# Kernel tuning notes

Measured on AMD Instinct MI355X. Metric: run time of the kernel, lower is better.

The kernel has to match this reference:

```python
import jax, jax.numpy as jnp
import numpy as np

B, C, CK, CV, W, H = 8, 256, 256, 256, 64, 64
EPS = 1e-6

def setup_inputs() -> dict:
    key = jax.random.key(0)
    ks = jax.random.split(key, 13)
    def wmat(k, shape, fan_in):
        return jax.random.normal(k, shape, jnp.float32) / np.float32(np.sqrt(fan_in))
    return {
        "x": jax.random.normal(ks[0], (B, C, W, H), jnp.float32),
        "qw": wmat(ks[1], (CK, C), C), "qb": jnp.zeros((CK,), jnp.float32),
        "kw": wmat(ks[2], (CK, C), C), "kb": jnp.zeros((CK,), jnp.float32),
        "vw": wmat(ks[3], (CV, C), C), "vb": jnp.zeros((CV,), jnp.float32),
        "rw": wmat(ks[4], (C, CV), CV), "rb": jnp.zeros((C,), jnp.float32),
        "c1w": wmat(ks[5], (C, C, 3, 3), C * 9), "c1b": jnp.zeros((C,), jnp.float32),
        "c2w": wmat(ks[6], (C, C, 3, 3), C * 9), "c2b": jnp.zeros((C,), jnp.float32),
    }

def reference(x, qw, qb, kw, kb, vw, vb, rw, rb, c1w, c1b, c2w, c2b):
    Bz, Cc, Wd, Hd = x.shape
    n = Wd * Hd
    xf = x.reshape(Bz, Cc, n)                                  # [b,c,n]
    Q = jnp.einsum('oc,bcn->bon', qw, xf) + qb[None, :, None]  # 1x1 conv
    K = jnp.einsum('oc,bcn->bon', kw, xf) + kb[None, :, None]
    V = jnp.einsum('oc,bcn->bon', vw, xf) + vb[None, :, None]
    # l2 norm over channel dim (per token), exactly as torch.norm(dim=-2)
    Qn = Q / jnp.linalg.norm(Q, axis=1, keepdims=True)
    Kn = K / jnp.linalg.norm(K, axis=1, keepdims=True)
    Qt = jnp.transpose(Qn, (0, 2, 1))                          # [b,n,ck]
    # head loops in the original sum over the full channel dim -> single einsum
    agg_dom = jnp.einsum('bnk,bk->bn', Qt, Kn.sum(-1))         # [b,n]
    denom = 1.0 / (n + agg_dom + EPS)                          # [b,n]
    vsum = V.sum(-1)                                           # [b,cv]
    kv = jnp.einsum('bkn,bcn->bkc', Kn, V)                     # K^T V, [b,ck,cv]
    qkv = jnp.einsum('bnk,bkc->bcn', Qt, kv)                   # [b,cv,n]
    wv = (vsum[:, :, None] + qkv) * denom[:, None, :]
    wv = wv.reshape(Bz, -1, Hd, Wd)                            # matches torch .view(b,cv,h,w)
    attn = jnp.einsum('oc,bchw->bohw', rw, wv) + rb[None, :, None, None]
    dn = ('NCHW', 'OIHW', 'NCHW')
    h = jax.lax.conv_general_dilated(attn, c1w, (1, 1), 'SAME', dimension_numbers=dn) + c1b[None, :, None, None]
    h = jax.lax.conv_general_dilated(h, c2w, (1, 1), 'SAME', dimension_numbers=dn) + c2b[None, :, None, None]
    return h * x + x
```

## Files before the change

### kernel.cpp

```cpp
#include <hip/hip_runtime.h>
#include <math.h>


typedef unsigned short u16;
typedef __attribute__((ext_vector_type(8))) short short8;
typedef __attribute__((ext_vector_type(4))) float f32x4;
typedef __attribute__((ext_vector_type(4))) unsigned short us4v;

#define ASYNC16(g, l) __builtin_amdgcn_global_load_lds( \
    (const __attribute__((address_space(1))) unsigned int*)(g), \
    (__attribute__((address_space(3))) unsigned int*)(l), 16, 0, 0)

static __device__ __forceinline__ float b2f(u16 h) {
  unsigned int u = ((unsigned int)h) << 16;
  return __builtin_bit_cast(float, u);
}
static __device__ __forceinline__ u16 f2b(float f) {
  unsigned int u = __builtin_bit_cast(unsigned int, f);
  u += 0x7fffu + ((u >> 16) & 1u);
  return (u16)(u >> 16);
}

#define NB 1048576L

__global__ __launch_bounds__(256) void prep1(
    const float* __restrict__ qw, const float* __restrict__ kw,
    const float* __restrict__ vw, const float* __restrict__ rw,
    const float* __restrict__ c1w, const float* __restrict__ c2w,
    const float* __restrict__ kb, const float* __restrict__ vb,
    u16* __restrict__ qw16, u16* __restrict__ kvw16, u16* __restrict__ rwT16,
    u16* __restrict__ wr1, u16* __restrict__ wr2,
    float* __restrict__ kvbias, float* __restrict__ zbuf)
{
  if (blockIdx.x == 5632) {
    int t = threadIdx.x;
    if (t < 256) { kvbias[t] = kb[t]; kvbias[t + 256] = vb[t]; }
    if (t < 64) zbuf[t] = 0.f;
    return;
  }
  long g = (long)blockIdx.x * 256 + threadIdx.x;
  if (g < 65536) {
    qw16[g] = f2b(qw[g]);
  } else if (g < 196608) {
    long e = g - 65536;
    kvw16[e] = f2b(e < 65536 ? kw[e] : vw[e - 65536]);
  } else if (g < 262144) {
    long e = g - 196608;
    int cv = e >> 8, co = e & 255;
    rwT16[e] = f2b(rw[co * 256 + cv]);
  } else if (g < 851968) {
    long e = g - 262144;
    int m = e / 2304, r = e - m * 2304;
    int d = r >> 8, c = r & 255;
    wr1[e] = f2b(c1w[m * 2304 + c * 9 + d]);
  } else {
    long e = g - 851968;
    int m = e / 2304, r = e - m * 2304;
    int d = r >> 8, c = r & 255;
    wr2[e] = f2b(c2w[m * 2304 + c * 9 + d]);
  }
}

__global__ __launch_bounds__(256) void prep_T(
    const float* __restrict__ c1w, const float* __restrict__ rb, float* __restrict__ T)
{
  int m = blockIdx.x, co = threadIdx.x;
  float r = rb[co];
  const float* p = c1w + (long)m * 2304 + co * 9;
  float lv[9];
#pragma unroll
  for (int d = 0; d < 9; d++) lv[d] = p[d] * r;
#pragma unroll
  for (int d = 0; d < 9; d++)
#pragma unroll
    for (int off = 32; off; off >>= 1) lv[d] += __shfl_down(lv[d], off, 64);
  __shared__ float red[4][9];
  int w = co >> 6, l = co & 63;
  if (l == 0)
#pragma unroll
    for (int d = 0; d < 9; d++) red[w][d] = lv[d];
  __syncthreads();
  if (co < 9) T[m * 9 + co] = red[0][co] + red[1][co] + red[2][co] + red[3][co];
}

__global__ __launch_bounds__(256) void corr_k(
    const float* __restrict__ T, const float* __restrict__ c1b, float* __restrict__ corr)
{
  int e = blockIdx.x * 256 + threadIdx.x;
  int m = e & 255, p = e >> 8;
  int y = p >> 6, xx = p & 63;
  float s = c1b[m];
#pragma unroll
  for (int d = 0; d < 9; d++) {
    int dy = d / 3 - 1, dx = d - (d / 3) * 3 - 1;
    if ((unsigned)(y + dy) < 64u && (unsigned)(xx + dx) < 64u) s += T[m * 9 + d];
  }
  corr[e] = s;
}

__global__ __launch_bounds__(256) void transposeX(
    const float* __restrict__ x, u16* __restrict__ xT)
{
  __shared__ float T[64][65];
  int n0 = blockIdx.x * 64, c0 = blockIdx.y * 64, b = blockIdx.z;
  int t = threadIdx.x;
#pragma unroll
  for (int i = 0; i < 4; i++) {
    int c = (t >> 4) + i * 16, nn = (t & 15) * 4;
    float4 v = *(const float4*)&x[(long)b * NB + (long)(c0 + c) * 4096 + n0 + nn];
    T[c][nn] = v.x; T[c][nn + 1] = v.y; T[c][nn + 2] = v.z; T[c][nn + 3] = v.w;
  }
  __syncthreads();
#pragma unroll
  for (int i = 0; i < 4; i++) {
    int n = (t >> 4) + i * 16, cc = (t & 15) * 4;
    us4v o;
#pragma unroll
    for (int e = 0; e < 4; e++) o[e] = f2b(T[cc + e][n]);
    *(us4v*)&xT[(long)b * NB + (long)(n0 + n) * 256 + c0 + cc] = o;
  }
}

__global__ __launch_bounds__(256) void gemm_nt(
    const u16* __restrict__ A, const u16* __restrict__ B, u16* __restrict__ out,
    int K, int lda, int ldb, long sAb, long sBb, long sOb, long sR, long sC,
    int mode, const float* __restrict__ p1, const float* __restrict__ p2)
{
  __shared__ __align__(16) u16 As[2][128 * 32];
  __shared__ __align__(16) u16 Bs[2][128 * 32];
  int b = blockIdx.z;
  long i0 = (long)blockIdx.y * 128;
  long j0 = (long)blockIdx.x * 128;
  const u16* Ab = A + b * sAb + i0 * lda;
  const u16* Bb = B + b * sBb + j0 * ldb;
  int t = threadIdx.x, wave = t >> 6, lane = t & 63;
  int wi = (wave >> 1) * 64, wj = (wave & 1) * 64;
  int li = lane & 15, quad = lane >> 4;
  int qs = (lane & 3) ^ ((lane >> 3) & 3);
  int qx = quad ^ ((lane >> 1) & 3);
  int r0 = (wave * 128 + lane) >> 2;
  int r1 = (wave * 128 + 64 + lane) >> 2;
  f32x4 acc[4][4];
#pragma unroll
  for (int i = 0; i < 4; i++)
#pragma unroll
    for (int j = 0; j < 4; j++) acc[i][j] = (f32x4){0.f, 0.f, 0.f, 0.f};

  auto STAGE = [&](int kc, int buf) {
    int k0 = kc * 32;
    ASYNC16(Ab + (long)r0 * lda + k0 + qs * 8, &As[buf][(wave * 128) * 8]);
    ASYNC16(Bb + (long)r0 * ldb + k0 + qs * 8, &Bs[buf][(wave * 128) * 8]);
    ASYNC16(Ab + (long)r1 * lda + k0 + qs * 8, &As[buf][(wave * 128 + 64) * 8]);
    ASYNC16(Bb + (long)r1 * ldb + k0 + qs * 8, &Bs[buf][(wave * 128 + 64) * 8]);
  };

  int nk = K >> 5, cur = 0;
  STAGE(0, 0);
#pragma unroll 1
  for (int kc = 0; kc < nk; kc++) {
    if (kc + 1 < nk) {
      STAGE(kc + 1, cur ^ 1);
      asm volatile("s_waitcnt vmcnt(4)" ::: "memory");
    } else {
      asm volatile("s_waitcnt vmcnt(0)" ::: "memory");
    }
    __builtin_amdgcn_s_barrier();
    const u16* as = &As[cur][0];
    const u16* bs = &Bs[cur][0];
    short8 af[4], bf[4];
#pragma unroll
    for (int s = 0; s < 4; s++) af[s] = *(const short8*)&as[(wi + s * 16 + li) * 32 + qx * 8];
#pragma unroll
    for (int s = 0; s < 4; s++) bf[s] = *(const short8*)&bs[(wj + s * 16 + li) * 32 + qx * 8];
#pragma unroll
    for (int si = 0; si < 4; si++)
#pragma unroll
      for (int sj = 0; sj < 4; sj++)
        acc[si][sj] = __builtin_amdgcn_mfma_f32_16x16x32_bf16(af[si], bf[sj], acc[si][sj], 0, 0, 0);
    __builtin_amdgcn_s_barrier();
    cur ^= 1;
  }

#pragma unroll
  for (int si = 0; si < 4; si++)
#pragma unroll
    for (int sj = 0; sj < 4; sj++) {
      long col = j0 + wj + sj * 16 + li;
#pragma unroll
      for (int r = 0; r < 4; r++) {
        long row = i0 + wi + si * 16 + quad * 4 + r;
        float v = acc[si][sj][r];
        if (mode == 0) {
          if (p1) v += p1[row];
          if (p2) v += p2[col];
        } else {
          v = (v + p1[b * 256 + col]) * p2[b * 4096 + row];
        }
        out[b * sOb + row * sR + col * sC] = f2b(v);
      }
    }
}

__global__ __launch_bounds__(256) void gemm_kv(
    const u16* __restrict__ KV, float* __restrict__ part)
{
  __shared__ __align__(16) u16 As[2][128 * 32];
  __shared__ __align__(16) u16 Bs[2][128 * 32];
  int z = blockIdx.z;
  int b = z & 7, sp = z >> 3;
  long i0 = (long)blockIdx.y * 128;
  long j0 = (long)blockIdx.x * 128;
  const u16* Ab = KV + (long)b * 2 * NB + i0 * 4096;
  const u16* Bb = KV + (long)b * 2 * NB + NB + j0 * 4096;
  int t = threadIdx.x, wave = t >> 6, lane = t & 63;
  int wi = (wave >> 1) * 64, wj = (wave & 1) * 64;
  int li = lane & 15, quad = lane >> 4;
  int qs = (lane & 3) ^ ((lane >> 3) & 3);
  int qx = quad ^ ((lane >> 1) & 3);
  int r0 = (wave * 128 + lane) >> 2;
  int r1 = (wave * 128 + 64 + lane) >> 2;
  f32x4 acc[4][4];
#pragma unroll
  for (int i = 0; i < 4; i++)
#pragma unroll
    for (int j = 0; j < 4; j++) acc[i][j] = (f32x4){0.f, 0.f, 0.f, 0.f};

  auto STAGE = [&](int kc, int buf) {
    int k0 = sp * 512 + kc * 32;
    ASYNC16(Ab + (long)r0 * 4096 + k0 + qs * 8, &As[buf][(wave * 128) * 8]);
    ASYNC16(Bb + (long)r0 * 4096 + k0 + qs * 8, &Bs[buf][(wave * 128) * 8]);
    ASYNC16(Ab + (long)r1 * 4096 + k0 + qs * 8, &As[buf][(wave * 128 + 64) * 8]);
    ASYNC16(Bb + (long)r1 * 4096 + k0 + qs * 8, &Bs[buf][(wave * 128 + 64) * 8]);
  };

  int cur = 0;
  STAGE(0, 0);
#pragma unroll 1
  for (int kc = 0; kc < 16; kc++) {
    if (kc + 1 < 16) {
      STAGE(kc + 1, cur ^ 1);
      asm volatile("s_waitcnt vmcnt(4)" ::: "memory");
    } else {
      asm volatile("s_waitcnt vmcnt(0)" ::: "memory");
    }
    __builtin_amdgcn_s_barrier();
    const u16* as = &As[cur][0];
    const u16* bs = &Bs[cur][0];
    short8 af[4], bf[4];
#pragma unroll
    for (int s = 0; s < 4; s++) af[s] = *(const short8*)&as[(wi + s * 16 + li) * 32 + qx * 8];
#pragma unroll
    for (int s = 0; s < 4; s++) bf[s] = *(const short8*)&bs[(wj + s * 16 + li) * 32 + qx * 8];
#pragma unroll
    for (int si = 0; si < 4; si++)
#pragma unroll
      for (int sj = 0; sj < 4; sj++)
        acc[si][sj] = __builtin_amdgcn_mfma_f32_16x16x32_bf16(af[si], bf[sj], acc[si][sj], 0, 0, 0);
    __builtin_amdgcn_s_barrier();
    cur ^= 1;
  }

  float* outp = part + ((long)sp * 8 + b) * 65536;
#pragma unroll
  for (int si = 0; si < 4; si++)
#pragma unroll
    for (int sj = 0; sj < 4; sj++) {
      long col = j0 + wj + sj * 16 + li;
#pragma unroll
      for (int r = 0; r < 4; r++) {
        long row = i0 + wi + si * 16 + quad * 4 + r;
        outp[col * 256 + row] = acc[si][sj][r];
      }
    }
}

__global__ __launch_bounds__(256) void reduce_kv(
    const float* __restrict__ part, u16* __restrict__ kvT)
{
  int g = blockIdx.x * 256 + threadIdx.x;
  float s = 0.f;
#pragma unroll
  for (int sp = 0; sp < 8; sp++) s += part[(long)sp * 524288 + g];
  kvT[g] = f2b(s);
}

__global__ __launch_bounds__(256) void normQden(
    u16* __restrict__ Qt, const float* __restrict__ ksum, float* __restrict__ den)
{
  int row = blockIdx.x * 4 + (threadIdx.x >> 6);
  int lane = threadIdx.x & 63;
  int b = row >> 12;
  u16* p = Qt + (long)row * 256 + lane * 4;
  us4v v = *(const us4v*)p;
  float f0 = b2f(v[0]), f1 = b2f(v[1]), f2 = b2f(v[2]), f3 = b2f(v[3]);
  float s = f0 * f0 + f1 * f1 + f2 * f2 + f3 * f3;
#pragma unroll
  for (int m = 32; m; m >>= 1) s += __shfl_xor(s, m, 64);
  float r = 1.0f / sqrtf(s);
  float o0 = f0 * r, o1 = f1 * r, o2 = f2 * r, o3 = f3 * r;
  us4v o;
  o[0] = f2b(o0); o[1] = f2b(o1); o[2] = f2b(o2); o[3] = f2b(o3);
  *(us4v*)p = o;
  float4 ks = *(const float4*)&ksum[b * 256 + lane * 4];
  float s2 = o0 * ks.x + o1 * ks.y + o2 * ks.z + o3 * ks.w;
#pragma unroll
  for (int m = 32; m; m >>= 1) s2 += __shfl_xor(s2, m, 64);
  if (lane == 0) den[row] = 1.0f / (4096.0f + s2 + 1e-6f);
}

__global__ __launch_bounds__(256) void sumsqK(
    const u16* __restrict__ KV, float* __restrict__ rsqK)
{
  __shared__ float red[16][68];
  int b = blockIdx.x >> 6, nc = blockIdx.x & 63;
  int n0 = nc * 64;
  int t = threadIdx.x;
  int nn = (t & 15) * 4, cg = t >> 4;
  const u16* base = KV + (long)b * 2 * NB;
  float s0 = 0.f, s1 = 0.f, s2 = 0.f, s3 = 0.f;
  for (int st = 0; st < 16; st++) {
    int c = cg + st * 16;
    us4v v = *(const us4v*)(base + (long)c * 4096 + n0 + nn);
    float a = b2f(v[0]), bb = b2f(v[1]), cc = b2f(v[2]), dd = b2f(v[3]);
    s0 = fmaf(a, a, s0); s1 = fmaf(bb, bb, s1);
    s2 = fmaf(cc, cc, s2); s3 = fmaf(dd, dd, s3);
  }
  red[cg][nn] = s0; red[cg][nn + 1] = s1; red[cg][nn + 2] = s2; red[cg][nn + 3] = s3;
  __syncthreads();
  if (t < 64) {
    float s = 0.f;
#pragma unroll
    for (int g = 0; g < 16; g++) s += red[g][t];
    rsqK[b * 4096 + n0 + t] = 1.0f / sqrtf(s);
  }
}

__global__ __launch_bounds__(256) void scale_sums(
    u16* __restrict__ KV, const float* __restrict__ rsqK,
    float* __restrict__ ksum, float* __restrict__ vsum)
{
  int z = blockIdx.x;
  int isV = z >> 11, rem = z & 2047, b = rem >> 8, c = rem & 255;
  u16* row = KV + (long)b * 2 * NB + (long)isV * NB + (long)c * 4096;
  const float* rq = rsqK + b * 4096;
  int t = threadIdx.x;
  float s = 0.f;
  short8 v0 = *(const short8*)&row[t * 16];
  short8 v1 = *(const short8*)&row[t * 16 + 8];
  if (!isV) {
    short8 o0, o1;
#pragma unroll
    for (int e = 0; e < 8; e++) {
      float a = b2f((u16)v0[e]) * rq[t * 16 + e];
      float bb = b2f((u16)v1[e]) * rq[t * 16 + 8 + e];
      s += a + bb;
      o0[e] = (short)f2b(a); o1[e] = (short)f2b(bb);
    }
    *(short8*)&row[t * 16] = o0;
    *(short8*)&row[t * 16 + 8] = o1;
  } else {
#pragma unroll
    for (int e = 0; e < 8; e++) s += b2f((u16)v0[e]) + b2f((u16)v1[e]);
  }
#pragma unroll
  for (int off = 32; off; off >>= 1) s += __shfl_down(s, off, 64);
  __shared__ float red[4];
  if ((t & 63) == 0) red[t >> 6] = s;
  __syncthreads();
  if (t == 0)
    (isV ? vsum : ksum)[b * 256 + c] = red[0] + red[1] + red[2] + red[3];
}

__global__ __launch_bounds__(512, 2) void conv_gemm(
    const u16* __restrict__ inT, const u16* __restrict__ wr,
    const float* __restrict__ cb, const float* __restrict__ xres,
    const float* __restrict__ zbuf,
    u16* __restrict__ out16, float* __restrict__ out32, int mode)
{
  __shared__ __align__(16) u16 S[2 * 24576];

  int lin = blockIdx.x;
  int b   = lin & 7;
  int n0  = (lin >> 3) * 128;

  int t = threadIdx.x, wave = t >> 6, lane = t & 63;
  int wm = (wave >> 1) * 64, wn = (wave & 1) * 64;
  int li = lane & 15, quad = lane >> 4;
  int qs8 = (lane & 7) ^ ((lane >> 3) & 7);
  const u16* inb = inT + (long)b * NB;

  int rr = wave * 8 + (lane >> 3);
  const u16* Ap0 = wr + (long)(rr)       * 2304 + qs8 * 8;
  const u16* Ap1 = wr + (long)(rr + 64)  * 2304 + qs8 * 8;
  const u16* Ap2 = wr + (long)(rr + 128) * 2304 + qs8 * 8;
  const u16* Ap3 = wr + (long)(rr + 192) * 2304 + qs8 * 8;
  const u16* Bp0 = inb + (long)(n0 + rr) * 256 + qs8 * 8;
  const u16* Bp1 = inb + (long)(n0 + 64 + rr) * 256 + qs8 * 8;
  const u16* zp  = (const u16*)zbuf + qs8 * 8;
  int yb0 = n0 >> 6, xb = rr;

  f32x4 acc[4][4];
#pragma unroll
  for (int i = 0; i < 4; i++)
#pragma unroll
    for (int j = 0; j < 4; j++) acc[i][j] = (f32x4){0.f, 0.f, 0.f, 0.f};

  auto STAGE = [&](int ks, int buf) {
    int d = ks >> 2;
    int dy = d / 3 - 1, dx = d - (d / 3) * 3 - 1;
    long shA = (long)ks * 64;
    long shB = (long)(dy * 64 + dx) * 256 + (ks & 3) * 64;
    u16* base = &S[buf * 24576];
    ASYNC16(Ap0 + shA, base + wave * 512);
    ASYNC16(Ap1 + shA, base + 4096 + wave * 512);
    ASYNC16(Ap2 + shA, base + 8192 + wave * 512);
    ASYNC16(Ap3 + shA, base + 12288 + wave * 512);
    bool v0 = ((unsigned)(yb0 + dy) < 64u) && ((unsigned)(xb + dx) < 64u);
    bool v1 = ((unsigned)(yb0 + 1 + dy) < 64u) && ((unsigned)(xb + dx) < 64u);
    ASYNC16(v0 ? Bp0 + shB : zp, base + 16384 + wave * 512);
    ASYNC16(v1 ? Bp1 + shB : zp, base + 20480 + wave * 512);
  };

  int cur = 0;
  STAGE(0, 0);
#pragma unroll 1
  for (int ks = 0; ks < 36; ks++) {
    if (ks + 1 < 36) {
      STAGE(ks + 1, cur ^ 1);
      asm volatile("s_waitcnt vmcnt(6)" ::: "memory");
    } else {
      asm volatile("s_waitcnt vmcnt(0)" ::: "memory");
    }
    __builtin_amdgcn_s_barrier();
    const u16* as = &S[cur * 24576];
    const u16* bs = as + 16384;
#pragma unroll
    for (int kk = 0; kk < 2; kk++) {
      short8 af[4], bf[4];
      int slot = (((kk << 2) | quad) ^ (lane & 7)) * 8;
#pragma unroll
      for (int s = 0; s < 4; s++) af[s] = *(const short8*)&as[(wm + s * 16 + li) * 64 + slot];
#pragma unroll
      for (int s = 0; s < 4; s++) bf[s] = *(const short8*)&bs[(wn + s * 16 + li) * 64 + slot];
#pragma unroll
      for (int si = 0; si < 4; si++)
#pragma unroll
        for (int sj = 0; sj < 4; sj++)
          acc[si][sj] = __builtin_amdgcn_mfma_f32_16x16x32_bf16(af[si], bf[sj], acc[si][sj], 0, 0, 0);
    }
    __builtin_amdgcn_s_barrier();
    cur ^= 1;
  }

#pragma unroll
  for (int si = 0; si < 4; si++)
#pragma unroll
    for (int sj = 0; sj < 4; sj++) {
      int n = n0 + wn + sj * 16 + li;
      int m0 = wm + si * 16 + quad * 4;
      if (mode == 0) {
        f32x4 c4 = *(const f32x4*)&cb[(long)n * 256 + m0];
        us4v o;
#pragma unroll
        for (int r = 0; r < 4; r++) o[r] = f2b(acc[si][sj][r] + c4[r]);
        *(us4v*)&out16[(long)b * NB + (long)n * 256 + m0] = o;
      } else {
#pragma unroll
        for (int r = 0; r < 4; r++) {
          int m = m0 + r;
          float v = acc[si][sj][r] + cb[m];
          long a = (long)b * NB + (long)m * 4096 + n;
          float xv = xres[a];
          out32[a] = fmaf(v, xv, xv);
        }
      }
    }
}

extern "C" void kernel_launch(void* const* d_in, const int* in_sizes, int n_in,
                              void* d_out, int out_size, void* d_ws, size_t ws_size,
                              hipStream_t stream)
{
  const float* x   = (const float*)d_in[0];
  const float* qw  = (const float*)d_in[1];
  const float* qb  = (const float*)d_in[2];
  const float* kw  = (const float*)d_in[3];
  const float* kb  = (const float*)d_in[4];
  const float* vw  = (const float*)d_in[5];
  const float* vb  = (const float*)d_in[6];
  const float* rw  = (const float*)d_in[7];
  const float* rb  = (const float*)d_in[8];
  const float* c1w = (const float*)d_in[9];
  const float* c1b = (const float*)d_in[10];
  const float* c2w = (const float*)d_in[11];
  const float* c2b = (const float*)d_in[12];

  u16* U     = (u16*)d_ws;
  u16* xT16  = U;
  u16* Qt16  = U + 8388608;
  u16* KV16  = U + 16777216;
  u16* wr2   = U + 33554432;
  u16* kvT16 = U + 34144256;
  float* Fws = (float*)(U + 34668544);
  float* ksum = Fws;
  float* vsum = Fws + 2048;
  float* zbuf = Fws + 4096;

  char* ob = (char*)d_out;
  float* kvpart = (float*)(ob + 0);
  float* den    = (float*)(ob + 16777216);
  float* rsqK   = (float*)(ob + 16908288);
  float* corr   = (float*)(ob + 17039360);
  u16*   w1p16  = (u16*)(ob + 21233664);
  u16*   wr1    = (u16*)(ob + 22413312);
  float* T      = (float*)(ob + 23592960);
  u16*   rwT16  = (u16*)(ob + 23629824);
  u16*   qw16   = (u16*)(ob + 23760896);
  u16*   kvw16  = (u16*)(ob + 23891968);
  float* kvbias = (float*)(ob + 24154112);
  float* outF   = (float*)d_out;

  u16* wvT16 = xT16;
  u16* h1T16 = Qt16;

  dim3 blk(256);

  prep1<<<5633, blk, 0, stream>>>(qw, kw, vw, rw, c1w, c2w, kb, vb,
                                  qw16, kvw16, rwT16, wr1, wr2, kvbias, zbuf);
  prep_T<<<256, blk, 0, stream>>>(c1w, rb, T);
  corr_k<<<4096, blk, 0, stream>>>(T, c1b, corr);
  transposeX<<<dim3(64, 4, 8), blk, 0, stream>>>(x, xT16);

  gemm_nt<<<dim3(2, 18, 1), blk, 0, stream>>>(wr1, rwT16, w1p16,
      256, 256, 256, 0L, 0L, 0L, 256L, 1L, 0, nullptr, nullptr);
  gemm_nt<<<dim3(2, 32, 8), blk, 0, stream>>>(xT16, qw16, Qt16,
      256, 256, 256, NB, 0L, NB, 256L, 1L, 0, nullptr, qb);
  gemm_nt<<<dim3(32, 4, 8), blk, 0, stream>>>(kvw16, xT16, KV16,
      256, 256, 256, 0L, NB, 2 * NB, 4096L, 1L, 0, kvbias, nullptr);

  sumsqK<<<512, blk, 0, stream>>>(KV16, rsqK);
  scale_sums<<<4096, blk, 0, stream>>>(KV16, rsqK, ksum, vsum);
  normQden<<<8192, blk, 0, stream>>>(Qt16, ksum, den);

  gemm_kv<<<dim3(2, 2, 64), blk, 0, stream>>>(KV16, kvpart);
  reduce_kv<<<2048, blk, 0, stream>>>(kvpart, kvT16);

  gemm_nt<<<dim3(2, 32, 8), blk, 0, stream>>>(Qt16, kvT16, wvT16,
      256, 256, 256, NB, 65536L, NB, 256L, 1L, 2, vsum, den);

  conv_gemm<<<256, 512, 0, stream>>>(wvT16, w1p16, corr, nullptr, zbuf,
                                     h1T16, nullptr, 0);
  conv_gemm<<<256, 512, 0, stream>>>(h1T16, wr2, c2b, x, zbuf,
                                     nullptr, outF, 1);
}
```

Before: 347.0 us.

## Fuse prep kernels, widen GEMM K-tile to 64, defer Q normalization to epilogue

The prep_T work is folded into prep1 as extra blocks, and corr_k and transposeX are merged into one launch, which removes kernel launches. The gemm_nt and gemm_kv kernels move from a 32-wide to a 64-wide K tile with a new XOR swizzle, halving loop iterations and barriers at the cost of doubled LDS use. Q normalization is no longer written back to Qt; qden stores only the per-row reciprocal norm, which the attention GEMM epilogue applies. This saves a read-modify-write pass over Qt but changes rounding, since unnormalized bf16 Q now enters the MFMA.

```diff
diff --git a/kernel.cpp b/kernel.cpp
--- a/kernel.cpp
+++ b/kernel.cpp
@@ -28,10 +28,31 @@
     const float* __restrict__ vw, const float* __restrict__ rw,
     const float* __restrict__ c1w, const float* __restrict__ c2w,
     const float* __restrict__ kb, const float* __restrict__ vb,
+    const float* __restrict__ rb,
     u16* __restrict__ qw16, u16* __restrict__ kvw16, u16* __restrict__ rwT16,
     u16* __restrict__ wr1, u16* __restrict__ wr2,
-    float* __restrict__ kvbias, float* __restrict__ zbuf)
-{
+    float* __restrict__ kvbias, float* __restrict__ zbuf, float* __restrict__ T)
+{
+  if (blockIdx.x >= 5633) {
+    int m = blockIdx.x - 5633, co = threadIdx.x;
+    float r = rb[co];
+    const float* p = c1w + (long)m * 2304 + co * 9;
+    float lv[9];
+#pragma unroll
+    for (int d = 0; d < 9; d++) lv[d] = p[d] * r;
+#pragma unroll
+    for (int d = 0; d < 9; d++)
+#pragma unroll
+      for (int off = 32; off; off >>= 1) lv[d] += __shfl_down(lv[d], off, 64);
+    __shared__ float red[4][9];
+    int w = co >> 6, l = co & 63;
+    if (l == 0)
+#pragma unroll
+      for (int d = 0; d < 9; d++) red[w][d] = lv[d];
+    __syncthreads();
+    if (co < 9) T[m * 9 + co] = red[0][co] + red[1][co] + red[2][co] + red[3][co];
+    return;
+  }
   if (blockIdx.x == 5632) {
     int t = threadIdx.x;
     if (t < 256) { kvbias[t] = kb[t]; kvbias[t + 256] = vb[t]; }
@@ -61,54 +82,33 @@
   }
 }
 
-__global__ __launch_bounds__(256) void prep_T(
-    const float* __restrict__ c1w, const float* __restrict__ rb, float* __restrict__ T)
-{
-  int m = blockIdx.x, co = threadIdx.x;
-  float r = rb[co];
-  const float* p = c1w + (long)m * 2304 + co * 9;
-  float lv[9];
-#pragma unroll
-  for (int d = 0; d < 9; d++) lv[d] = p[d] * r;
-#pragma unroll
-  for (int d = 0; d < 9; d++)
-#pragma unroll
-    for (int off = 32; off; off >>= 1) lv[d] += __shfl_down(lv[d], off, 64);
-  __shared__ float red[4][9];
-  int w = co >> 6, l = co & 63;
-  if (l == 0)
-#pragma unroll
-    for (int d = 0; d < 9; d++) red[w][d] = lv[d];
-  __syncthreads();
-  if (co < 9) T[m * 9 + co] = red[0][co] + red[1][co] + red[2][co] + red[3][co];
-}
-
-__global__ __launch_bounds__(256) void corr_k(
-    const float* __restrict__ T, const float* __restrict__ c1b, float* __restrict__ corr)
-{
-  int e = blockIdx.x * 256 + threadIdx.x;
-  int m = e & 255, p = e >> 8;
-  int y = p >> 6, xx = p & 63;
-  float s = c1b[m];
-#pragma unroll
-  for (int d = 0; d < 9; d++) {
-    int dy = d / 3 - 1, dx = d - (d / 3) * 3 - 1;
-    if ((unsigned)(y + dy) < 64u && (unsigned)(xx + dx) < 64u) s += T[m * 9 + d];
-  }
-  corr[e] = s;
-}
-
-__global__ __launch_bounds__(256) void transposeX(
+__global__ __launch_bounds__(256) void corr_transX(
+    const float* __restrict__ T, const float* __restrict__ c1b,
+    float* __restrict__ corr,
     const float* __restrict__ x, u16* __restrict__ xT)
 {
-  __shared__ float T[64][65];
-  int n0 = blockIdx.x * 64, c0 = blockIdx.y * 64, b = blockIdx.z;
-  int t = threadIdx.x;
+  __shared__ float Tl[64][65];
+  int bb = blockIdx.x, t = threadIdx.x;
+  if (bb < 4096) {
+    int e = bb * 256 + t;
+    int m = e & 255, p = e >> 8;
+    int y = p >> 6, xx = p & 63;
+    float s = c1b[m];
+#pragma unroll
+    for (int d = 0; d < 9; d++) {
+      int dy = d / 3 - 1, dx = d - (d / 3) * 3 - 1;
+      if ((unsigned)(y + dy) < 64u && (unsigned)(xx + dx) < 64u) s += T[m * 9 + d];
+    }
+    corr[e] = s;
+    return;
+  }
+  int lin = bb - 4096;
+  int n0 = (lin & 63) * 64, c0 = ((lin >> 6) & 3) * 64, b = lin >> 8;
 #pragma unroll
   for (int i = 0; i < 4; i++) {
     int c = (t >> 4) + i * 16, nn = (t & 15) * 4;
     float4 v = *(const float4*)&x[(long)b * NB + (long)(c0 + c) * 4096 + n0 + nn];
-    T[c][nn] = v.x; T[c][nn + 1] = v.y; T[c][nn + 2] = v.z; T[c][nn + 3] = v.w;
+    Tl[c][nn] = v.x; Tl[c][nn + 1] = v.y; Tl[c][nn + 2] = v.z; Tl[c][nn + 3] = v.w;
   }
   __syncthreads();
 #pragma unroll
@@ -116,7 +116,7 @@
     int n = (t >> 4) + i * 16, cc = (t & 15) * 4;
     us4v o;
 #pragma unroll
-    for (int e = 0; e < 4; e++) o[e] = f2b(T[cc + e][n]);
+    for (int e = 0; e < 4; e++) o[e] = f2b(Tl[cc + e][n]);
     *(us4v*)&xT[(long)b * NB + (long)(n0 + n) * 256 + c0 + cc] = o;
   }
 }
@@ -124,10 +124,11 @@
 __global__ __launch_bounds__(256) void gemm_nt(
     const u16* __restrict__ A, const u16* __restrict__ B, u16* __restrict__ out,
     int K, int lda, int ldb, long sAb, long sBb, long sOb, long sR, long sC,
-    int mode, const float* __restrict__ p1, const float* __restrict__ p2)
-{
-  __shared__ __align__(16) u16 As[2][128 * 32];
-  __shared__ __align__(16) u16 Bs[2][128 * 32];
+    int mode, const float* __restrict__ p1, const float* __restrict__ p2,
+    const float* __restrict__ p3)
+{
+  __shared__ __align__(16) u16 As[2][128 * 64];
+  __shared__ __align__(16) u16 Bs[2][128 * 64];
   int b = blockIdx.z;
   long i0 = (long)blockIdx.y * 128;
   long j0 = (long)blockIdx.x * 128;
@@ -136,10 +137,7 @@
   int t = threadIdx.x, wave = t >> 6, lane = t & 63;
   int wi = (wave >> 1) * 64, wj = (wave & 1) * 64;
   int li = lane & 15, quad = lane >> 4;
-  int qs = (lane & 3) ^ ((lane >> 3) & 3);
-  int qx = quad ^ ((lane >> 1) & 3);
-  int r0 = (wave * 128 + lane) >> 2;
-  int r1 = (wave * 128 + 64 + lane) >> 2;
+  int qs8 = (lane & 7) ^ ((lane >> 3) & 7);
   f32x4 acc[4][4];
 #pragma unroll
   for (int i = 0; i < 4; i++)
@@ -147,36 +145,42 @@
     for (int j = 0; j < 4; j++) acc[i][j] = (f32x4){0.f, 0.f, 0.f, 0.f};
 
   auto STAGE = [&](int kc, int buf) {
-    int k0 = kc * 32;
-    ASYNC16(Ab + (long)r0 * lda + k0 + qs * 8, &As[buf][(wave * 128) * 8]);
-    ASYNC16(Bb + (long)r0 * ldb + k0 + qs * 8, &Bs[buf][(wave * 128) * 8]);
-    ASYNC16(Ab + (long)r1 * lda + k0 + qs * 8, &As[buf][(wave * 128 + 64) * 8]);
-    ASYNC16(Bb + (long)r1 * ldb + k0 + qs * 8, &Bs[buf][(wave * 128 + 64) * 8]);
+    long k0 = (long)kc * 64 + qs8 * 8;
+#pragma unroll
+    for (int j = 0; j < 4; j++) {
+      int row = (wave * 4 + j) * 8 + (lane >> 3);
+      ASYNC16(Ab + (long)row * lda + k0, &As[buf][(wave * 4 + j) * 512]);
+      ASYNC16(Bb + (long)row * ldb + k0, &Bs[buf][(wave * 4 + j) * 512]);
+    }
   };
 
-  int nk = K >> 5, cur = 0;
+  int nk = K >> 6, cur = 0;
   STAGE(0, 0);
 #pragma unroll 1
   for (int kc = 0; kc < nk; kc++) {
     if (kc + 1 < nk) {
       STAGE(kc + 1, cur ^ 1);
-      asm volatile("s_waitcnt vmcnt(4)" ::: "memory");
+      asm volatile("s_waitcnt vmcnt(8)" ::: "memory");
     } else {
       asm volatile("s_waitcnt vmcnt(0)" ::: "memory");
     }
     __builtin_amdgcn_s_barrier();
     const u16* as = &As[cur][0];
     const u16* bs = &Bs[cur][0];
-    short8 af[4], bf[4];
-#pragma unroll
-    for (int s = 0; s < 4; s++) af[s] = *(const short8*)&as[(wi + s * 16 + li) * 32 + qx * 8];
-#pragma unroll
-    for (int s = 0; s < 4; s++) bf[s] = *(const short8*)&bs[(wj + s * 16 + li) * 32 + qx * 8];
-#pragma unroll
-    for (int si = 0; si < 4; si++)
-#pragma unroll
-      for (int sj = 0; sj < 4; sj++)
-        acc[si][sj] = __builtin_amdgcn_mfma_f32_16x16x32_bf16(af[si], bf[sj], acc[si][sj], 0, 0, 0);
+#pragma unroll
+    for (int kk = 0; kk < 2; kk++) {
+      short8 af[4], bf[4];
+      int slot = (((kk << 2) | quad) ^ (li & 7)) * 8;
+#pragma unroll
+      for (int s = 0; s < 4; s++) af[s] = *(const short8*)&as[(wi + s * 16 + li) * 64 + slot];
+#pragma unroll
+      for (int s = 0; s < 4; s++) bf[s] = *(const short8*)&bs[(wj + s * 16 + li) * 64 + slot];
+#pragma unroll
+      for (int si = 0; si < 4; si++)
+#pragma unroll
+        for (int sj = 0; sj < 4; sj++)
+          acc[si][sj] = __builtin_amdgcn_mfma_f32_16x16x32_bf16(af[si], bf[sj], acc[si][sj], 0, 0, 0);
+    }
     __builtin_amdgcn_s_barrier();
     cur ^= 1;
   }
@@ -194,7 +198,7 @@
           if (p1) v += p1[row];
           if (p2) v += p2[col];
         } else {
-          v = (v + p1[b * 256 + col]) * p2[b * 4096 + row];
+          v = (v * p3[b * 4096 + row] + p1[b * 256 + col]) * p2[b * 4096 + row];
         }
         out[b * sOb + row * sR + col * sC] = f2b(v);
       }
@@ -204,8 +208,8 @@
 __global__ __launch_bounds__(256) void gemm_kv(
     const u16* __restrict__ KV, float* __restrict__ part)
 {
-  __shared__ __align__(16) u16 As[2][128 * 32];
-  __shared__ __align__(16) u16 Bs[2][128 * 32];
+  __shared__ __align__(16) u16 As[2][128 * 64];
+  __shared__ __align__(16) u16 Bs[2][128 * 64];
   int z = blockIdx.z;
   int b = z & 7, sp = z >> 3;
   long i0 = (long)blockIdx.y * 128;
@@ -215,10 +219,7 @@
   int t = threadIdx.x, wave = t >> 6, lane = t & 63;
   int wi = (wave >> 1) * 64, wj = (wave & 1) * 64;
   int li = lane & 15, quad = lane >> 4;
-  int qs = (lane & 3) ^ ((lane >> 3) & 3);
-  int qx = quad ^ ((lane >> 1) & 3);
-  int r0 = (wave * 128 + lane) >> 2;
-  int r1 = (wave * 128 + 64 + lane) >> 2;
+  int qs8 = (lane & 7) ^ ((lane >> 3) & 7);
   f32x4 acc[4][4];
 #pragma unroll
   for (int i = 0; i < 4; i++)
@@ -226,36 +227,42 @@
     for (int j = 0; j < 4; j++) acc[i][j] = (f32x4){0.f, 0.f, 0.f, 0.f};
 
   auto STAGE = [&](int kc, int buf) {
-    int k0 = sp * 512 + kc * 32;
-    ASYNC16(Ab + (long)r0 * 4096 + k0 + qs * 8, &As[buf][(wave * 128) * 8]);
-    ASYNC16(Bb + (long)r0 * 4096 + k0 + qs * 8, &Bs[buf][(wave * 128) * 8]);
-    ASYNC16(Ab + (long)r1 * 4096 + k0 + qs * 8, &As[buf][(wave * 128 + 64) * 8]);
-    ASYNC16(Bb + (long)r1 * 4096 + k0 + qs * 8, &Bs[buf][(wave * 128 + 64) * 8]);
+    long k0 = (long)sp * 512 + kc * 64 + qs8 * 8;
+#pragma unroll
+    for (int j = 0; j < 4; j++) {
+      int row = (wave * 4 + j) * 8 + (lane >> 3);
+      ASYNC16(Ab + (long)row * 4096 + k0, &As[buf][(wave * 4 + j) * 512]);
+      ASYNC16(Bb + (long)row * 4096 + k0, &Bs[buf][(wave * 4 + j) * 512]);
+    }
   };
 
   int cur = 0;
   STAGE(0, 0);
 #pragma unroll 1
-  for (int kc = 0; kc < 16; kc++) {
-    if (kc + 1 < 16) {
+  for (int kc = 0; kc < 8; kc++) {
+    if (kc + 1 < 8) {
       STAGE(kc + 1, cur ^ 1);
-      asm volatile("s_waitcnt vmcnt(4)" ::: "memory");
+      asm volatile("s_waitcnt vmcnt(8)" ::: "memory");
     } else {
       asm volatile("s_waitcnt vmcnt(0)" ::: "memory");
     }
     __builtin_amdgcn_s_barrier();
     const u16* as = &As[cur][0];
     const u16* bs = &Bs[cur][0];
-    short8 af[4], bf[4];
-#pragma unroll
-    for (int s = 0; s < 4; s++) af[s] = *(const short8*)&as[(wi + s * 16 + li) * 32 + qx * 8];
-#pragma unroll
-    for (int s = 0; s < 4; s++) bf[s] = *(const short8*)&bs[(wj + s * 16 + li) * 32 + qx * 8];
-#pragma unroll
-    for (int si = 0; si < 4; si++)
-#pragma unroll
-      for (int sj = 0; sj < 4; sj++)
-        acc[si][sj] = __builtin_amdgcn_mfma_f32_16x16x32_bf16(af[si], bf[sj], acc[si][sj], 0, 0, 0);
+#pragma unroll
+    for (int kk = 0; kk < 2; kk++) {
+      short8 af[4], bf[4];
+      int slot = (((kk << 2) | quad) ^ (li & 7)) * 8;
+#pragma unroll
+      for (int s = 0; s < 4; s++) af[s] = *(const short8*)&as[(wi + s * 16 + li) * 64 + slot];
+#pragma unroll
+      for (int s = 0; s < 4; s++) bf[s] = *(const short8*)&bs[(wj + s * 16 + li) * 64 + slot];
+#pragma unroll
+      for (int si = 0; si < 4; si++)
+#pragma unroll
+        for (int sj = 0; sj < 4; sj++)
+          acc[si][sj] = __builtin_amdgcn_mfma_f32_16x16x32_bf16(af[si], bf[sj], acc[si][sj], 0, 0, 0);
+    }
     __builtin_amdgcn_s_barrier();
     cur ^= 1;
   }
@@ -284,28 +291,28 @@
   kvT[g] = f2b(s);
 }
 
-__global__ __launch_bounds__(256) void normQden(
-    u16* __restrict__ Qt, const float* __restrict__ ksum, float* __restrict__ den)
+__global__ __launch_bounds__(256) void qden(
+    const u16* __restrict__ Qt, const float* __restrict__ ksum,
+    float* __restrict__ rq, float* __restrict__ den)
 {
   int row = blockIdx.x * 4 + (threadIdx.x >> 6);
   int lane = threadIdx.x & 63;
   int b = row >> 12;
-  u16* p = Qt + (long)row * 256 + lane * 4;
-  us4v v = *(const us4v*)p;
+  us4v v = *(const us4v*)(Qt + (long)row * 256 + lane * 4);
+  float4 ks = *(const float4*)&ksum[b * 256 + lane * 4];
   float f0 = b2f(v[0]), f1 = b2f(v[1]), f2 = b2f(v[2]), f3 = b2f(v[3]);
   float s = f0 * f0 + f1 * f1 + f2 * f2 + f3 * f3;
-#pragma unroll
-  for (int m = 32; m; m >>= 1) s += __shfl_xor(s, m, 64);
-  float r = 1.0f / sqrtf(s);
-  float o0 = f0 * r, o1 = f1 * r, o2 = f2 * r, o3 = f3 * r;
-  us4v o;
-  o[0] = f2b(o0); o[1] = f2b(o1); o[2] = f2b(o2); o[3] = f2b(o3);
-  *(us4v*)p = o;
-  float4 ks = *(const float4*)&ksum[b * 256 + lane * 4];
-  float s2 = o0 * ks.x + o1 * ks.y + o2 * ks.z + o3 * ks.w;
-#pragma unroll
-  for (int m = 32; m; m >>= 1) s2 += __shfl_xor(s2, m, 64);
-  if (lane == 0) den[row] = 1.0f / (4096.0f + s2 + 1e-6f);
+  float s2 = f0 * ks.x + f1 * ks.y + f2 * ks.z + f3 * ks.w;
+#pragma unroll
+  for (int m = 32; m; m >>= 1) {
+    s += __shfl_xor(s, m, 64);
+    s2 += __shfl_xor(s2, m, 64);
+  }
+  if (lane == 0) {
+    float r = 1.0f / sqrtf(s);
+    rq[row] = r;
+    den[row] = 1.0f / (4096.0f + s2 * r + 1e-6f);
+  }
 }
 
 __global__ __launch_bounds__(256) void sumsqK(
@@ -518,6 +525,7 @@
   u16*   qw16   = (u16*)(ob + 23760896);
   u16*   kvw16  = (u16*)(ob + 23891968);
   float* kvbias = (float*)(ob + 24154112);
+  float* rq     = (float*)(ob + 24158208);
   float* outF   = (float*)d_out;
 
   u16* wvT16 = xT16;
@@ -525,28 +533,26 @@
 
   dim3 blk(256);
 
-  prep1<<<5633, blk, 0, stream>>>(qw, kw, vw, rw, c1w, c2w, kb, vb,
-                                  qw16, kvw16, rwT16, wr1, wr2, kvbias, zbuf);
-  prep_T<<<256, blk, 0, stream>>>(c1w, rb, T);
-  corr_k<<<4096, blk, 0, stream>>>(T, c1b, corr);
-  transposeX<<<dim3(64, 4, 8), blk, 0, stream>>>(x, xT16);
+  prep1<<<5889, blk, 0, stream>>>(qw, kw, vw, rw, c1w, c2w, kb, vb, rb,
+                                  qw16, kvw16, rwT16, wr1, wr2, kvbias, zbuf, T);
+  corr_transX<<<6144, blk, 0, stream>>>(T, c1b, corr, x, xT16);
 
   gemm_nt<<<dim3(2, 18, 1), blk, 0, stream>>>(wr1, rwT16, w1p16,
-      256, 256, 256, 0L, 0L, 0L, 256L, 1L, 0, nullptr, nullptr);
+      256, 256, 256, 0L, 0L, 0L, 256L, 1L, 0, nullptr, nullptr, nullptr);
   gemm_nt<<<dim3(2, 32, 8), blk, 0, stream>>>(xT16, qw16, Qt16,
-      256, 256, 256, NB, 0L, NB, 256L, 1L, 0, nullptr, qb);
+      256, 256, 256, NB, 0L, NB, 256L, 1L, 0, nullptr, qb, nullptr);
   gemm_nt<<<dim3(32, 4, 8), blk, 0, stream>>>(kvw16, xT16, KV16,
-      256, 256, 256, 0L, NB, 2 * NB, 4096L, 1L, 0, kvbias, nullptr);
+      256, 256, 256, 0L, NB, 2 * NB, 4096L, 1L, 0, kvbias, nullptr, nullptr);
 
   sumsqK<<<512, blk, 0, stream>>>(KV16, rsqK);
   scale_sums<<<4096, blk, 0, stream>>>(KV16, rsqK, ksum, vsum);
-  normQden<<<8192, blk, 0, stream>>>(Qt16, ksum, den);
+  qden<<<8192, blk, 0, stream>>>(Qt16, ksum, rq, den);
 
   gemm_kv<<<dim3(2, 2, 64), blk, 0, stream>>>(KV16, kvpart);
   reduce_kv<<<2048, blk, 0, stream>>>(kvpart, kvT16);
 
   gemm_nt<<<dim3(2, 32, 8), blk, 0, stream>>>(Qt16, kvT16, wvT16,
-      256, 256, 256, NB, 65536L, NB, 256L, 1L, 2, vsum, den);
+      256, 256, 256, NB, 65536L, NB, 256L, 1L, 2, vsum, den, rq);
 
   conv_gemm<<<256, 512, 0, stream>>>(wvT16, w1p16, corr, nullptr, zbuf,
                                      h1T16, nullptr, 0);
```

Measured after the change: 339.9 us. 1.02x faster.
